# Optimization experiments

Measured on AMD Instinct MI355X. Metric: run time of the kernel, lower is better.

Reference implementation:

```python
import jax, jax.numpy as jnp
import numpy as np

EPS = 1e-5

def _layernorm(x, g, b):
    m = jnp.mean(x, axis=-1, keepdims=True)
    v = jnp.mean((x - m) ** 2, axis=-1, keepdims=True)
    return (x - m) * jax.lax.rsqrt(v + EPS) * g + b

def setup_inputs() -> dict:
    key = jax.random.key(0)
    ks = jax.random.split(key, 6)
    b, s, n = 1, 256, 512
    dim_msa, dim_pair, heads, dim_head = 64, 128, 8, 32
    dim_inner = heads * dim_head
    msa = jax.random.normal(ks[0], (b, s, n, dim_msa), dtype=jnp.float32)
    pairwise_repr = jax.random.normal(ks[1], (b, n, n, dim_pair), dtype=jnp.float32)
    mask = jnp.ones((b, n), dtype=bool)
    return {
        "msa": msa,
        "pairwise_repr": pairwise_repr,
        "ln_msa_g": jnp.ones((dim_msa,), jnp.float32),
        "ln_msa_b": jnp.zeros((dim_msa,), jnp.float32),
        "W_vg": jax.random.normal(ks[2], (dim_msa, dim_inner * 2), jnp.float32) * 0.02,
        "ln_pair_g": jnp.ones((dim_pair,), jnp.float32),
        "ln_pair_b": jnp.zeros((dim_pair,), jnp.float32),
        "W_pair": jax.random.normal(ks[3], (dim_pair, heads), jnp.float32) * 0.02,
        "W_out": jax.random.normal(ks[4], (dim_inner, dim_msa), jnp.float32) * 0.02,
        "mask": mask,
    }

def reference(msa, pairwise_repr, ln_msa_g, ln_msa_b, W_vg, ln_pair_g, ln_pair_b, W_pair, W_out, mask):
    heads, dim_head = 8, 32
    b, s, n, dim_msa = msa.shape
    # values and gates: LN -> LinearNoBias -> split (gv h d)
    vg = _layernorm(msa, ln_msa_g, ln_msa_b) @ W_vg            # [b,s,n,2*h*d]
    vg = vg.reshape(b, s, n, 2, heads, dim_head)
    vg = jnp.transpose(vg, (3, 0, 4, 1, 2, 5))                  # [2,b,h,s,n,d]
    values, gates = vg[0], jax.nn.sigmoid(vg[1])
    # pair bias: LN -> LinearNoBias -> [b,h,i,j]
    bias = _layernorm(pairwise_repr, ln_pair_g, ln_pair_b) @ W_pair  # [b,i,j,h]
    bias = jnp.transpose(bias, (0, 3, 1, 2))                    # [b,h,i,j]
    bias = jnp.where(mask[:, None, None, :], bias, -jnp.inf)
    weights = jax.nn.softmax(bias, axis=-1)                     # [b,h,i,j]
    out = jnp.einsum('bhij,bhsjd->bhsid', weights, values)      # [b,h,s,n,d]
    out = out * gates
    out = jnp.transpose(out, (0, 2, 3, 1, 4)).reshape(b, s, n, heads * dim_head)
    return out @ W_out                                          # [b,s,n,dim_msa]
```

## Files before the change

kernel.cpp:

```cpp
#include <hip/hip_runtime.h>
#include <hip/hip_bf16.h>


#define S 256
#define N 512
#define DM 64
#define DP 128
#define H 8
#define C 256
#define ROWS (S * N)

typedef __attribute__((ext_vector_type(8))) short bf16x8;
typedef __attribute__((ext_vector_type(4))) float f32x4;

static __device__ __forceinline__ float bf2f(unsigned int u16) {
    union { unsigned int i; float f; } x;
    x.i = u16 << 16;
    return x.f;
}
static __device__ __forceinline__ unsigned short f2bf(float f) {
    union { float f; unsigned int i; } x;
    x.f = f;
    unsigned int r = x.i + 0x7FFFu + ((x.i >> 16) & 1u);
    return (unsigned short)(r >> 16);
}
static __device__ __forceinline__ void gload16(const void* g, void* l) {
    __builtin_amdgcn_global_load_lds(
        (const __attribute__((address_space(1))) void*)g,
        (__attribute__((address_space(3))) void*)l, 16, 0, 0);
}

__global__ __launch_bounds__(256) void k0_prep(
    const float* __restrict__ Wvg, const float* __restrict__ g, const float* __restrict__ b,
    const float* __restrict__ Wout, const float* __restrict__ gp, const float* __restrict__ bp,
    const float* __restrict__ Wp,
    unsigned short* __restrict__ WTvg, float* __restrict__ biasvg, unsigned short* __restrict__ WoutT,
    float* __restrict__ Wg, float* __restrict__ sgcb)
{
    const int t = threadIdx.x;
    if (blockIdx.x < 2) {
        const int c = blockIdx.x * 256 + t;
        float bias = 0.f;
        unsigned short row[64];
#pragma unroll
        for (int k = 0; k < 64; k++) {
            const float w = Wvg[k * 512 + c];
            row[k] = f2bf(w * g[k]);
            bias = fmaf(w, b[k], bias);
        }
#pragma unroll
        for (int q = 0; q < 8; q++) *(uint4*)(WTvg + c * 64 + q * 8) = *(const uint4*)(row + q * 8);
        biasvg[c] = bias;
    } else if (blockIdx.x == 2) {
        const int m = t >> 2, c0 = (t & 3) * 64;
        unsigned short row[64];
#pragma unroll
        for (int q = 0; q < 64; q++) row[q] = f2bf(Wout[(c0 + q) * 64 + m]);
#pragma unroll
        for (int q = 0; q < 8; q++) *(uint4*)(WoutT + m * 256 + c0 + q * 8) = *(const uint4*)(row + q * 8);
    } else {
        if (t < 128) {
            const float gm = gp[t];
#pragma unroll
            for (int h = 0; h < 8; h++) Wg[t * 8 + h] = gm * Wp[t * 8 + h];
        } else if (t < 136) {
            const int h = t - 128;
            float sg = 0.f, cb = 0.f;
            for (int k = 0; k < 128; k++) {
                sg = fmaf(gp[k], Wp[k * 8 + h], sg);
                cb = fmaf(bp[k], Wp[k * 8 + h], cb);
            }
            sgcb[h] = sg;
            sgcb[8 + h] = cb;
        }
    }
}

__global__ __launch_bounds__(512, 4) void k1_vg_mfma(
    const float* __restrict__ msa, const unsigned short* __restrict__ WTvg,
    const float* __restrict__ biasvg,
    unsigned short* __restrict__ VT, unsigned short* __restrict__ G)
{
    __shared__ unsigned short wt[512 * 64];
    __shared__ unsigned short at[64 * 64];
    const int t = threadIdx.x, lane = t & 63, w = t >> 6;
    const int l15 = lane & 15, lgrp = lane >> 4;
    const int s = blockIdx.x >> 1;
    const int jbase = (blockIdx.x & 1) * 256;

#pragma unroll
    for (int q = 0; q < 8; q++) {
        const int u = q * 512 + t;
        const int c = u >> 3, ch = u & 7;
        const uint4 v = *(const uint4*)(WTvg + c * 64 + ch * 8);
        *(uint4*)((char*)wt + c * 128 + ((ch ^ (c & 7)) * 16)) = v;
    }
    float biasr[4];
    float bias2[4][4];
    if (w < 4) {
#pragma unroll
        for (int cf = 0; cf < 4; cf++) biasr[cf] = biasvg[w * 64 + cf * 16 + l15];
    } else {
#pragma unroll
        for (int cf = 0; cf < 4; cf++)
#pragma unroll
            for (int r = 0; r < 4; r++) bias2[cf][r] = biasvg[w * 64 + cf * 16 + lgrp * 4 + r];
    }

    for (int tile = 0; tile < 4; ++tile) {
        const int j0 = jbase + tile * 64;
        {
            const int r = t >> 3, kc = (t & 7) * 8;
            const float* src = msa + ((size_t)(s * 512 + j0 + r)) * 64 + kc;
            const float4 x0 = *(const float4*)src;
            const float4 x1 = *(const float4*)(src + 4);
            float s1 = x0.x + x0.y + x0.z + x0.w + x1.x + x1.y + x1.z + x1.w;
            float s2 = x0.x * x0.x + x0.y * x0.y + x0.z * x0.z + x0.w * x0.w
                     + x1.x * x1.x + x1.y * x1.y + x1.z * x1.z + x1.w * x1.w;
#pragma unroll
            for (int off = 1; off < 8; off <<= 1) {
                s1 += __shfl_xor(s1, off);
                s2 += __shfl_xor(s2, off);
            }
            const float m = s1 * (1.f / 64.f);
            const float inv = rsqrtf(s2 * (1.f / 64.f) - m * m + 1e-5f);
            unsigned short buf[8];
            buf[0] = f2bf((x0.x - m) * inv); buf[1] = f2bf((x0.y - m) * inv);
            buf[2] = f2bf((x0.z - m) * inv); buf[3] = f2bf((x0.w - m) * inv);
            buf[4] = f2bf((x1.x - m) * inv); buf[5] = f2bf((x1.y - m) * inv);
            buf[6] = f2bf((x1.z - m) * inv); buf[7] = f2bf((x1.w - m) * inv);
            *(uint4*)((char*)at + r * 128 + (((t & 7) ^ (r & 7)) * 16)) = *(const uint4*)buf;
        }
        __syncthreads();

        f32x4 acc[4][4];
#pragma unroll
        for (int rf = 0; rf < 4; rf++)
#pragma unroll
            for (int cf = 0; cf < 4; cf++) acc[rf][cf] = (f32x4){0.f, 0.f, 0.f, 0.f};

#pragma unroll
        for (int ks = 0; ks < 2; ks++) {
            bf16x8 bfr[4];
#pragma unroll
            for (int cf = 0; cf < 4; cf++) {
                const int c = w * 64 + cf * 16 + l15;
                bfr[cf] = *(const bf16x8*)((const char*)wt + c * 128 + (((ks * 4 + lgrp) ^ (c & 7)) * 16));
            }
#pragma unroll
            for (int rf = 0; rf < 4; rf++) {
                const int rr = rf * 16 + l15;
                const bf16x8 afr = *(const bf16x8*)((const char*)at + rr * 128 + (((ks * 4 + lgrp) ^ (rr & 7)) * 16));
                if (w < 4) {
#pragma unroll
                    for (int cf = 0; cf < 4; cf++)
                        acc[rf][cf] = __builtin_amdgcn_mfma_f32_16x16x32_bf16(afr, bfr[cf], acc[rf][cf], 0, 0, 0);
                } else {
#pragma unroll
                    for (int cf = 0; cf < 4; cf++)
                        acc[rf][cf] = __builtin_amdgcn_mfma_f32_16x16x32_bf16(bfr[cf], afr, acc[rf][cf], 0, 0, 0);
                }
            }
        }
        __syncthreads();

        if (w < 4) {
#pragma unroll
            for (int rf = 0; rf < 4; rf++)
#pragma unroll
                for (int cf = 0; cf < 4; cf++) {
                    const int c = w * 64 + cf * 16 + l15;
                    const int j = j0 + rf * 16 + lgrp * 4;
                    uint2 o;
                    o.x = (unsigned)f2bf(acc[rf][cf][0] + biasr[cf]) |
                          ((unsigned)f2bf(acc[rf][cf][1] + biasr[cf]) << 16);
                    o.y = (unsigned)f2bf(acc[rf][cf][2] + biasr[cf]) |
                          ((unsigned)f2bf(acc[rf][cf][3] + biasr[cf]) << 16);
                    *(uint2*)(VT + ((size_t)s * C + c) * N + j) = o;
                }
        } else {
#pragma unroll
            for (int rf = 0; rf < 4; rf++)
#pragma unroll
                for (int cf = 0; cf < 4; cf++) {
                    const int j = j0 + rf * 16 + l15;
                    const int cp = (w - 4) * 64 + cf * 16 + lgrp * 4;
                    float sg[4];
#pragma unroll
                    for (int r = 0; r < 4; r++)
                        sg[r] = 1.f / (1.f + __expf(-(acc[rf][cf][r] + bias2[cf][r])));
                    uint2 o;
                    o.x = (unsigned)f2bf(sg[0]) | ((unsigned)f2bf(sg[1]) << 16);
                    o.y = (unsigned)f2bf(sg[2]) | ((unsigned)f2bf(sg[3]) << 16);
                    *(uint2*)(G + ((size_t)(s * 512 + j)) * C + cp) = o;
                }
        }
    }
}

__global__ __launch_bounds__(512) void k2_bias_softmax(
    const float* __restrict__ pair, const float* __restrict__ Wg,
    const float* __restrict__ sgcb, unsigned short* __restrict__ Wt)
{
    __shared__ float bias_lds[H][N];
    const int i = blockIdx.x;
    const int t = threadIdx.x;
    const int sub = t & 15, rgrp = t >> 4;

    float wreg[2][4][8];
#pragma unroll
    for (int q = 0; q < 2; q++)
#pragma unroll
        for (int c = 0; c < 4; c++) {
            const int k = (q * 16 + sub) * 4 + c;
            const float4 w0 = *(const float4*)(Wg + k * 8);
            const float4 w1 = *(const float4*)(Wg + k * 8 + 4);
            wreg[q][c][0] = w0.x; wreg[q][c][1] = w0.y; wreg[q][c][2] = w0.z; wreg[q][c][3] = w0.w;
            wreg[q][c][4] = w1.x; wreg[q][c][5] = w1.y; wreg[q][c][6] = w1.z; wreg[q][c][7] = w1.w;
        }
    float sgr[8], cbr[8];
#pragma unroll
    for (int h = 0; h < 8; h++) { sgr[h] = sgcb[h]; cbr[h] = sgcb[8 + h]; }

    for (int pass = 0; pass < 16; ++pass) {
        const int r = pass * 32 + rgrp;
        const float* px = pair + ((size_t)i * N + r) * DP;
        const float4 x0 = *(const float4*)(px + (0 * 16 + sub) * 4);
        const float4 x1 = *(const float4*)(px + (1 * 16 + sub) * 4);
        float s1 = x0.x + x0.y + x0.z + x0.w + x1.x + x1.y + x1.z + x1.w;
        float s2 = x0.x * x0.x + x0.y * x0.y + x0.z * x0.z + x0.w * x0.w
                 + x1.x * x1.x + x1.y * x1.y + x1.z * x1.z + x1.w * x1.w;
#pragma unroll
        for (int off = 1; off < 16; off <<= 1) {
            s1 += __shfl_xor(s1, off);
            s2 += __shfl_xor(s2, off);
        }
        const float m = s1 * (1.f / 128.f);
        const float inv = rsqrtf(s2 * (1.f / 128.f) - m * m + 1e-5f);

        float dots[8];
#pragma unroll
        for (int h = 0; h < 8; h++) dots[h] = 0.f;
        const float xs[2][4] = {{x0.x, x0.y, x0.z, x0.w}, {x1.x, x1.y, x1.z, x1.w}};
#pragma unroll
        for (int q = 0; q < 2; q++)
#pragma unroll
            for (int c = 0; c < 4; c++)
#pragma unroll
                for (int h = 0; h < 8; h++) dots[h] = fmaf(xs[q][c], wreg[q][c][h], dots[h]);
#pragma unroll
        for (int off = 1; off < 16; off <<= 1)
#pragma unroll
            for (int h = 0; h < 8; h++) dots[h] += __shfl_xor(dots[h], off);

        if (sub == 0) {
#pragma unroll
            for (int h = 0; h < 8; h++)
                bias_lds[h][r] = inv * (dots[h] - m * sgr[h]) + cbr[h];
        }
    }
    __syncthreads();

    const int lane = t & 63, h = t >> 6;
    float v[8];
    float mx = -1e30f;
#pragma unroll
    for (int q = 0; q < 8; q++) {
        v[q] = bias_lds[h][q * 64 + lane];
        mx = fmaxf(mx, v[q]);
    }
#pragma unroll
    for (int off = 32; off > 0; off >>= 1) mx = fmaxf(mx, __shfl_xor(mx, off));
    float sum = 0.f;
#pragma unroll
    for (int q = 0; q < 8; q++) {
        v[q] = __expf(v[q] - mx);
        sum += v[q];
    }
#pragma unroll
    for (int off = 32; off > 0; off >>= 1) sum += __shfl_xor(sum, off);
    const float rs = 1.f / sum;
#pragma unroll
    for (int q = 0; q < 8; q++)
        Wt[((size_t)h * N + i) * N + q * 64 + lane] = f2bf(v[q] * rs);
}

__global__ __launch_bounds__(256, 2) void k3_einsum_h(
    const unsigned short* __restrict__ Wt, const unsigned short* __restrict__ VT,
    unsigned short* __restrict__ G)
{
    __shared__ unsigned short a_lds[2][128 * 64];
    __shared__ unsigned short b_lds[2][128 * 64];
    const int raw = blockIdx.x;
    const int bid = (raw & 7) * 256 + (raw >> 3);
    const int h = bid >> 8;
    const int rem = bid & 255;
    const int nb = rem >> 2, ib = rem & 3;
    const int n0 = nb * 128, i0 = ib * 128;
    const int t = threadIdx.x, lane = t & 63, w = t >> 6;
    const int l15 = lane & 15, lgrp = lane >> 4;
    const int wr = w >> 1, wc = w & 1;

    const unsigned short* srcA[4];
    const unsigned short* srcB[4];
    int dst[4];
#pragma unroll
    for (int q = 0; q < 4; ++q) {
        const int slot = q * 256 + t;
        const int row = slot >> 3, chp = slot & 7;
        const int ch = chp ^ (row & 7);
        const int n = n0 + row;
        srcA[q] = VT + ((size_t)((n >> 5) * 256 + h * 32 + (n & 31))) * 512 + ch * 8;
        srcB[q] = Wt + ((size_t)(h * 512 + i0 + row)) * 512 + ch * 8;
        dst[q] = slot * 16;
    }

#define K3_STAGE(P, J0)                                                    \
    {                                                                      \
        _Pragma("unroll")                                                  \
        for (int q = 0; q < 4; ++q)                                        \
            gload16(srcA[q] + (J0), (char*)a_lds[P] + dst[q]);             \
        _Pragma("unroll")                                                  \
        for (int q = 0; q < 4; ++q)                                        \
            gload16(srcB[q] + (J0), (char*)b_lds[P] + dst[q]);             \
    }

    f32x4 acc[4][4];
#pragma unroll
    for (int fn = 0; fn < 4; fn++)
#pragma unroll
        for (int fi = 0; fi < 4; fi++) acc[fn][fi] = (f32x4){0.f, 0.f, 0.f, 0.f};

    K3_STAGE(0, 0);

    for (int kt = 0; kt < 8; ++kt) {
        const int cur = kt & 1;
        if (kt < 7) {
            K3_STAGE(cur ^ 1, (kt + 1) * 64);
            asm volatile("s_waitcnt vmcnt(8)" ::: "memory");
        } else {
            asm volatile("s_waitcnt vmcnt(0)" ::: "memory");
        }
        __builtin_amdgcn_s_barrier();
#pragma unroll
        for (int ks = 0; ks < 2; ++ks) {
            bf16x8 af[4], bf[4];
#pragma unroll
            for (int f = 0; f < 4; ++f) {
                const int ra = wr * 64 + f * 16 + l15;
                af[f] = *(const bf16x8*)((const char*)a_lds[cur] + ra * 128 + (((ks * 4 + lgrp) ^ (ra & 7)) * 16));
                const int rb = wc * 64 + f * 16 + l15;
                bf[f] = *(const bf16x8*)((const char*)b_lds[cur] + rb * 128 + (((ks * 4 + lgrp) ^ (rb & 7)) * 16));
            }
#pragma unroll
            for (int fn = 0; fn < 4; ++fn)
#pragma unroll
                for (int fi = 0; fi < 4; ++fi)
                    acc[fn][fi] = __builtin_amdgcn_mfma_f32_16x16x32_bf16(af[fn], bf[fi], acc[fn][fi], 0, 0, 0);
        }
        __builtin_amdgcn_s_barrier();
    }
#undef K3_STAGE

#pragma unroll
    for (int fn = 0; fn < 4; ++fn) {
        const int nl = n0 + wr * 64 + fn * 16 + lgrp * 4;
        const int s = nl >> 5, d = nl & 31;
#pragma unroll
        for (int fi = 0; fi < 4; ++fi) {
            const int i = i0 + wc * 64 + fi * 16 + l15;
            const size_t base = ((size_t)(s * 512 + i)) * 256 + h * 32 + d;
            const uint2 u = *(const uint2*)(G + base);
            const float g0 = bf2f(u.x & 0xFFFFu), g1 = bf2f(u.x >> 16);
            const float g2 = bf2f(u.y & 0xFFFFu), g3 = bf2f(u.y >> 16);
            uint2 o;
            o.x = (unsigned)f2bf(acc[fn][fi][0] * g0) | ((unsigned)f2bf(acc[fn][fi][1] * g1) << 16);
            o.y = (unsigned)f2bf(acc[fn][fi][2] * g2) | ((unsigned)f2bf(acc[fn][fi][3] * g3) << 16);
            *(uint2*)(G + base) = o;
        }
    }
}

__global__ __launch_bounds__(256, 4) void k4_out(
    const unsigned short* __restrict__ gated, const unsigned short* __restrict__ WoutT,
    float* __restrict__ out)
{
    __shared__ unsigned short w_lds[64 * 256];
    __shared__ unsigned short a_lds[64 * 256];
    const int t = threadIdx.x, lane = t & 63, w = t >> 6;
    const int l15 = lane & 15, lgrp = lane >> 4;
    const size_t r0 = (size_t)blockIdx.x * 64;

#pragma unroll
    for (int q = 0; q < 8; ++q) {
        const int u = q * 256 + t;
        const int row = u >> 5, kc = u & 31;
        const uint4 v = *(const uint4*)(WoutT + row * 256 + kc * 8);
        *(uint4*)((char*)w_lds + row * 512 + ((kc ^ (row & 31)) * 16)) = v;
    }
#pragma unroll
    for (int q = 0; q < 8; ++q) {
        const int slot = q * 256 + t;
        const int row = slot >> 5, chp = slot & 31;
        const int ch = chp ^ (row & 31);
        gload16(gated + (r0 + row) * 256 + ch * 8,
                (char*)a_lds + (q * 256 + (t & 192)) * 16);
    }
    __syncthreads();

    f32x4 acc[4];
#pragma unroll
    for (int fm = 0; fm < 4; fm++) acc[fm] = (f32x4){0.f, 0.f, 0.f, 0.f};
#pragma unroll
    for (int ks = 0; ks < 8; ++ks) {
        const int ra = w * 16 + l15;
        const bf16x8 af = *(const bf16x8*)((const char*)a_lds + ra * 512 + (((ks * 4 + lgrp) ^ (ra & 31)) * 16));
#pragma unroll
        for (int fm = 0; fm < 4; ++fm) {
            const int rm = fm * 16 + l15;
            const bf16x8 bf = *(const bf16x8*)((const char*)w_lds + rm * 512 + (((ks * 4 + lgrp) ^ (rm & 31)) * 16));
            acc[fm] = __builtin_amdgcn_mfma_f32_16x16x32_bf16(af, bf, acc[fm], 0, 0, 0);
        }
    }
#pragma unroll
    for (int fm = 0; fm < 4; ++fm)
#pragma unroll
        for (int r = 0; r < 4; ++r)
            out[(r0 + w * 16 + lgrp * 4 + r) * 64 + fm * 16 + l15] = acc[fm][r];
}

extern "C" void kernel_launch(void* const* d_in, const int* in_sizes, int n_in,
                              void* d_out, int out_size, void* d_ws, size_t ws_size,
                              hipStream_t stream) {
    (void)in_sizes; (void)n_in; (void)out_size; (void)ws_size;
    const float* msa       = (const float*)d_in[0];
    const float* pair      = (const float*)d_in[1];
    const float* ln_msa_g  = (const float*)d_in[2];
    const float* ln_msa_b  = (const float*)d_in[3];
    const float* W_vg      = (const float*)d_in[4];
    const float* ln_pair_g = (const float*)d_in[5];
    const float* ln_pair_b = (const float*)d_in[6];
    const float* W_pair    = (const float*)d_in[7];
    const float* W_out     = (const float*)d_in[8];
    float* out = (float*)d_out;

    char* ws = (char*)d_ws;
    size_t off = 0;
    unsigned short* VT    = (unsigned short*)(ws + off); off += (size_t)ROWS * C * 2;
    unsigned short* G     = (unsigned short*)(ws + off); off += (size_t)ROWS * C * 2;
    unsigned short* Wt    = (unsigned short*)(ws + off); off += (size_t)H * N * N * 2;
    unsigned short* WTvg  = (unsigned short*)(ws + off); off += 512 * 64 * 2;
    float*          biasvg = (float*)(ws + off); off += 512 * 4;
    unsigned short* WoutT = (unsigned short*)(ws + off); off += 64 * 256 * 2;
    float*          Wg    = (float*)(ws + off); off += 128 * 8 * 4;
    float*          sgcb  = (float*)(ws + off); off += 16 * 4;

    k0_prep<<<4, 256, 0, stream>>>(W_vg, ln_msa_g, ln_msa_b, W_out, ln_pair_g, ln_pair_b, W_pair,
                                   WTvg, biasvg, WoutT, Wg, sgcb);
    k1_vg_mfma<<<512, 512, 0, stream>>>(msa, WTvg, biasvg, VT, G);
    k2_bias_softmax<<<512, 512, 0, stream>>>(pair, Wg, sgcb, Wt);
    k3_einsum_h<<<2048, 256, 0, stream>>>(Wt, VT, G);
    k4_out<<<2048, 256, 0, stream>>>(G, WoutT, out);
}
```

Baseline: 215.8 us.

## Loop all heads inside each einsum block to reuse VT/G spatial locality

The einsum kernel now assigns each block two s-rows by 128 i-columns and iterates over all 8 heads in a 64-step pipelined loop, writing gated output per head. Gate values are prefetched at the start of each head. The grid shrinks from 2048 to 512 blocks and the A tile halves, so each block has less MFMA work per step but a longer pipeline. The softmax kernel is also launched before the value/gate projection, so VT and G are likely still in cache when the einsum reads them. The risk is lower parallelism (512 blocks) and more per-head epilogue stalls.

```diff
diff --git a/kernel.cpp b/kernel.cpp
--- a/kernel.cpp
+++ b/kernel.cpp
@@ -289,96 +289,127 @@
     const unsigned short* __restrict__ Wt, const unsigned short* __restrict__ VT,
     unsigned short* __restrict__ G)
 {
-    __shared__ unsigned short a_lds[2][128 * 64];
+    __shared__ unsigned short a_lds[2][64 * 64];
     __shared__ unsigned short b_lds[2][128 * 64];
     const int raw = blockIdx.x;
-    const int bid = (raw & 7) * 256 + (raw >> 3);
-    const int h = bid >> 8;
-    const int rem = bid & 255;
-    const int nb = rem >> 2, ib = rem & 3;
-    const int n0 = nb * 128, i0 = ib * 128;
+    const int bid = (raw & 7) * 64 + (raw >> 3);
+    const int nb = bid >> 2;
+    const int ib = bid & 3;
+    const int s0 = nb * 2;
+    const int i0 = ib * 128;
     const int t = threadIdx.x, lane = t & 63, w = t >> 6;
     const int l15 = lane & 15, lgrp = lane >> 4;
     const int wr = w >> 1, wc = w & 1;
 
-    const unsigned short* srcA[4];
+    const unsigned short* srcA[2];
     const unsigned short* srcB[4];
-    int dst[4];
+    int dstA[2], dstB[4];
+#pragma unroll
+    for (int q = 0; q < 2; ++q) {
+        const int slot = q * 256 + t;
+        const int row = slot >> 3, chp = slot & 7;
+        const int ch = chp ^ (row & 7);
+        const int s = s0 + (row >> 5);
+        srcA[q] = VT + ((size_t)(s * 256 + (row & 31))) * 512 + ch * 8;
+        dstA[q] = slot * 16;
+    }
 #pragma unroll
     for (int q = 0; q < 4; ++q) {
         const int slot = q * 256 + t;
         const int row = slot >> 3, chp = slot & 7;
         const int ch = chp ^ (row & 7);
-        const int n = n0 + row;
-        srcA[q] = VT + ((size_t)((n >> 5) * 256 + h * 32 + (n & 31))) * 512 + ch * 8;
-        srcB[q] = Wt + ((size_t)(h * 512 + i0 + row)) * 512 + ch * 8;
-        dst[q] = slot * 16;
-    }
-
-#define K3_STAGE(P, J0)                                                    \
-    {                                                                      \
-        _Pragma("unroll")                                                  \
-        for (int q = 0; q < 4; ++q)                                        \
-            gload16(srcA[q] + (J0), (char*)a_lds[P] + dst[q]);             \
-        _Pragma("unroll")                                                  \
-        for (int q = 0; q < 4; ++q)                                        \
-            gload16(srcB[q] + (J0), (char*)b_lds[P] + dst[q]);             \
-    }
-
-    f32x4 acc[4][4];
-#pragma unroll
-    for (int fn = 0; fn < 4; fn++)
+        srcB[q] = Wt + ((size_t)(i0 + row)) * 512 + ch * 8;
+        dstB[q] = slot * 16;
+    }
+
+#define K3_STAGE(P, U)                                                          \
+    {                                                                           \
+        const int hh_ = (U) >> 3, kk_ = (U) & 7;                                \
+        const int offA_ = hh_ * 16384 + kk_ * 64;                               \
+        const int offB_ = hh_ * 262144 + kk_ * 64;                              \
+        _Pragma("unroll")                                                       \
+        for (int q = 0; q < 2; ++q) gload16(srcA[q] + offA_, (char*)a_lds[P] + dstA[q]); \
+        _Pragma("unroll")                                                       \
+        for (int q = 0; q < 4; ++q) gload16(srcB[q] + offB_, (char*)b_lds[P] + dstB[q]); \
+    }
+
+    f32x4 acc[2][4];
+#pragma unroll
+    for (int fn = 0; fn < 2; fn++)
 #pragma unroll
         for (int fi = 0; fi < 4; fi++) acc[fn][fi] = (f32x4){0.f, 0.f, 0.f, 0.f};
+    uint2 gpre[2][4];
 
     K3_STAGE(0, 0);
 
-    for (int kt = 0; kt < 8; ++kt) {
-        const int cur = kt & 1;
-        if (kt < 7) {
-            K3_STAGE(cur ^ 1, (kt + 1) * 64);
-            asm volatile("s_waitcnt vmcnt(8)" ::: "memory");
+    for (int u = 0; u < 64; ++u) {
+        const int cur = u & 1;
+        if (u < 63) {
+            K3_STAGE(cur ^ 1, u + 1);
+            asm volatile("s_waitcnt vmcnt(6)" ::: "memory");
         } else {
             asm volatile("s_waitcnt vmcnt(0)" ::: "memory");
         }
         __builtin_amdgcn_s_barrier();
+
+        if ((u & 7) == 0) {
+            const int h = u >> 3;
+#pragma unroll
+            for (int fn = 0; fn < 2; ++fn) {
+                const int nl = wr * 32 + fn * 16 + lgrp * 4;
+                const int s = s0 + (nl >> 5), d = nl & 31;
+#pragma unroll
+                for (int fi = 0; fi < 4; ++fi) {
+                    const int i = i0 + wc * 64 + fi * 16 + l15;
+                    gpre[fn][fi] = *(const uint2*)(G + ((size_t)(s * 512 + i)) * 256 + h * 32 + d);
+                }
+            }
+        }
+
 #pragma unroll
         for (int ks = 0; ks < 2; ++ks) {
-            bf16x8 af[4], bf[4];
+            bf16x8 af[2], bf[4];
+#pragma unroll
+            for (int f = 0; f < 2; ++f) {
+                const int ra = wr * 32 + f * 16 + l15;
+                af[f] = *(const bf16x8*)((const char*)a_lds[cur] + ra * 128 + (((ks * 4 + lgrp) ^ (ra & 7)) * 16));
+            }
 #pragma unroll
             for (int f = 0; f < 4; ++f) {
-                const int ra = wr * 64 + f * 16 + l15;
-                af[f] = *(const bf16x8*)((const char*)a_lds[cur] + ra * 128 + (((ks * 4 + lgrp) ^ (ra & 7)) * 16));
                 const int rb = wc * 64 + f * 16 + l15;
                 bf[f] = *(const bf16x8*)((const char*)b_lds[cur] + rb * 128 + (((ks * 4 + lgrp) ^ (rb & 7)) * 16));
             }
 #pragma unroll
-            for (int fn = 0; fn < 4; ++fn)
+            for (int fn = 0; fn < 2; ++fn)
 #pragma unroll
                 for (int fi = 0; fi < 4; ++fi)
                     acc[fn][fi] = __builtin_amdgcn_mfma_f32_16x16x32_bf16(af[fn], bf[fi], acc[fn][fi], 0, 0, 0);
         }
         __builtin_amdgcn_s_barrier();
+
+        if ((u & 7) == 7) {
+            const int h = u >> 3;
+#pragma unroll
+            for (int fn = 0; fn < 2; ++fn) {
+                const int nl = wr * 32 + fn * 16 + lgrp * 4;
+                const int s = s0 + (nl >> 5), d = nl & 31;
+#pragma unroll
+                for (int fi = 0; fi < 4; ++fi) {
+                    const int i = i0 + wc * 64 + fi * 16 + l15;
+                    const size_t base = ((size_t)(s * 512 + i)) * 256 + h * 32 + d;
+                    const uint2 uu = gpre[fn][fi];
+                    const float g0 = bf2f(uu.x & 0xFFFFu), g1 = bf2f(uu.x >> 16);
+                    const float g2 = bf2f(uu.y & 0xFFFFu), g3 = bf2f(uu.y >> 16);
+                    uint2 o;
+                    o.x = (unsigned)f2bf(acc[fn][fi][0] * g0) | ((unsigned)f2bf(acc[fn][fi][1] * g1) << 16);
+                    o.y = (unsigned)f2bf(acc[fn][fi][2] * g2) | ((unsigned)f2bf(acc[fn][fi][3] * g3) << 16);
+                    *(uint2*)(G + base) = o;
+                    acc[fn][fi] = (f32x4){0.f, 0.f, 0.f, 0.f};
+                }
+            }
+        }
     }
 #undef K3_STAGE
-
-#pragma unroll
-    for (int fn = 0; fn < 4; ++fn) {
-        const int nl = n0 + wr * 64 + fn * 16 + lgrp * 4;
-        const int s = nl >> 5, d = nl & 31;
-#pragma unroll
-        for (int fi = 0; fi < 4; ++fi) {
-            const int i = i0 + wc * 64 + fi * 16 + l15;
-            const size_t base = ((size_t)(s * 512 + i)) * 256 + h * 32 + d;
-            const uint2 u = *(const uint2*)(G + base);
-            const float g0 = bf2f(u.x & 0xFFFFu), g1 = bf2f(u.x >> 16);
-            const float g2 = bf2f(u.y & 0xFFFFu), g3 = bf2f(u.y >> 16);
-            uint2 o;
-            o.x = (unsigned)f2bf(acc[fn][fi][0] * g0) | ((unsigned)f2bf(acc[fn][fi][1] * g1) << 16);
-            o.y = (unsigned)f2bf(acc[fn][fi][2] * g2) | ((unsigned)f2bf(acc[fn][fi][3] * g3) << 16);
-            *(uint2*)(G + base) = o;
-        }
-    }
 }
 
 __global__ __launch_bounds__(256, 4) void k4_out(
@@ -457,8 +488,8 @@
 
     k0_prep<<<4, 256, 0, stream>>>(W_vg, ln_msa_g, ln_msa_b, W_out, ln_pair_g, ln_pair_b, W_pair,
                                    WTvg, biasvg, WoutT, Wg, sgcb);
+    k2_bias_softmax<<<512, 512, 0, stream>>>(pair, Wg, sgcb, Wt);
     k1_vg_mfma<<<512, 512, 0, stream>>>(msa, WTvg, biasvg, VT, G);
-    k2_bias_softmax<<<512, 512, 0, stream>>>(pair, Wg, sgcb, Wt);
-    k3_einsum_h<<<2048, 256, 0, stream>>>(Wt, VT, G);
+    k3_einsum_h<<<512, 256, 0, stream>>>(Wt, VT, G);
     k4_out<<<2048, 256, 0, stream>>>(G, WoutT, out);
 }
```

New measurement: 224.4 us. 1.04x slower.

## Enlarge einsum tile to 128x256 and drop double buffering in k3

Applied to the files above, without the earlier changes.

The einsum kernel now computes a 128(n) x 256(i) tile per block instead of 128x128, so each V tile is reused across twice as many output columns and the grid halves to 1024 blocks. LDS double buffering is replaced by a single-buffer load/sync/compute/sync loop with 48KB LDS, and each wave holds 4x8 accumulator fragments. The softmax kernel is also launched before the vg projection. Register pressure rises (128 accumulator floats per lane) and losing the prefetch overlap may expose global load latency, since launch_bounds still asks for 2 blocks per CU.

```diff
diff --git a/kernel.cpp b/kernel.cpp
--- a/kernel.cpp
+++ b/kernel.cpp
@@ -289,21 +289,21 @@
     const unsigned short* __restrict__ Wt, const unsigned short* __restrict__ VT,
     unsigned short* __restrict__ G)
 {
-    __shared__ unsigned short a_lds[2][128 * 64];
-    __shared__ unsigned short b_lds[2][128 * 64];
+    __shared__ unsigned short a_lds[128 * 64];
+    __shared__ unsigned short b_lds[256 * 64];
     const int raw = blockIdx.x;
-    const int bid = (raw & 7) * 256 + (raw >> 3);
-    const int h = bid >> 8;
-    const int rem = bid & 255;
-    const int nb = rem >> 2, ib = rem & 3;
-    const int n0 = nb * 128, i0 = ib * 128;
+    const int bid = (raw & 7) * 128 + (raw >> 3);
+    const int h = bid >> 7;
+    const int rem = bid & 127;
+    const int nb = rem >> 1, ib = rem & 1;
+    const int n0 = nb * 128, i0 = ib * 256;
     const int t = threadIdx.x, lane = t & 63, w = t >> 6;
     const int l15 = lane & 15, lgrp = lane >> 4;
-    const int wr = w >> 1, wc = w & 1;
+    const int wn = w >> 1, wi = w & 1;
 
     const unsigned short* srcA[4];
-    const unsigned short* srcB[4];
-    int dst[4];
+    const unsigned short* srcB[8];
+    int dstA[4], dstB[8];
 #pragma unroll
     for (int q = 0; q < 4; ++q) {
         const int slot = q * 256 + t;
@@ -311,68 +311,65 @@
         const int ch = chp ^ (row & 7);
         const int n = n0 + row;
         srcA[q] = VT + ((size_t)((n >> 5) * 256 + h * 32 + (n & 31))) * 512 + ch * 8;
+        dstA[q] = slot * 16;
+    }
+#pragma unroll
+    for (int q = 0; q < 8; ++q) {
+        const int slot = q * 256 + t;
+        const int row = slot >> 3, chp = slot & 7;
+        const int ch = chp ^ (row & 7);
         srcB[q] = Wt + ((size_t)(h * 512 + i0 + row)) * 512 + ch * 8;
-        dst[q] = slot * 16;
-    }
-
-#define K3_STAGE(P, J0)                                                    \
-    {                                                                      \
-        _Pragma("unroll")                                                  \
-        for (int q = 0; q < 4; ++q)                                        \
-            gload16(srcA[q] + (J0), (char*)a_lds[P] + dst[q]);             \
-        _Pragma("unroll")                                                  \
-        for (int q = 0; q < 4; ++q)                                        \
-            gload16(srcB[q] + (J0), (char*)b_lds[P] + dst[q]);             \
-    }
-
-    f32x4 acc[4][4];
+        dstB[q] = slot * 16;
+    }
+
+    f32x4 acc[4][8];
 #pragma unroll
     for (int fn = 0; fn < 4; fn++)
 #pragma unroll
-        for (int fi = 0; fi < 4; fi++) acc[fn][fi] = (f32x4){0.f, 0.f, 0.f, 0.f};
-
-    K3_STAGE(0, 0);
+        for (int fi = 0; fi < 8; fi++) acc[fn][fi] = (f32x4){0.f, 0.f, 0.f, 0.f};
 
     for (int kt = 0; kt < 8; ++kt) {
-        const int cur = kt & 1;
-        if (kt < 7) {
-            K3_STAGE(cur ^ 1, (kt + 1) * 64);
-            asm volatile("s_waitcnt vmcnt(8)" ::: "memory");
-        } else {
-            asm volatile("s_waitcnt vmcnt(0)" ::: "memory");
-        }
-        __builtin_amdgcn_s_barrier();
+        const int j0 = kt * 64;
+#pragma unroll
+        for (int q = 0; q < 4; ++q) gload16(srcA[q] + j0, (char*)a_lds + dstA[q]);
+#pragma unroll
+        for (int q = 0; q < 8; ++q) gload16(srcB[q] + j0, (char*)b_lds + dstB[q]);
+        __syncthreads();
+
 #pragma unroll
         for (int ks = 0; ks < 2; ++ks) {
-            bf16x8 af[4], bf[4];
-#pragma unroll
-            for (int f = 0; f < 4; ++f) {
-                const int ra = wr * 64 + f * 16 + l15;
-                af[f] = *(const bf16x8*)((const char*)a_lds[cur] + ra * 128 + (((ks * 4 + lgrp) ^ (ra & 7)) * 16));
-                const int rb = wc * 64 + f * 16 + l15;
-                bf[f] = *(const bf16x8*)((const char*)b_lds[cur] + rb * 128 + (((ks * 4 + lgrp) ^ (rb & 7)) * 16));
+            bf16x8 af[4];
+#pragma unroll
+            for (int fn = 0; fn < 4; ++fn) {
+                const int ra = wn * 64 + fn * 16 + l15;
+                af[fn] = *(const bf16x8*)((const char*)a_lds + ra * 128 + (((ks * 4 + lgrp) ^ (ra & 7)) * 16));
+            }
+            bf16x8 bf[8];
+#pragma unroll
+            for (int fi = 0; fi < 8; ++fi) {
+                const int rb = wi * 128 + fi * 16 + l15;
+                bf[fi] = *(const bf16x8*)((const char*)b_lds + rb * 128 + (((ks * 4 + lgrp) ^ (rb & 7)) * 16));
             }
 #pragma unroll
             for (int fn = 0; fn < 4; ++fn)
 #pragma unroll
-                for (int fi = 0; fi < 4; ++fi)
+                for (int fi = 0; fi < 8; ++fi)
                     acc[fn][fi] = __builtin_amdgcn_mfma_f32_16x16x32_bf16(af[fn], bf[fi], acc[fn][fi], 0, 0, 0);
         }
-        __builtin_amdgcn_s_barrier();
-    }
-#undef K3_STAGE
+        __syncthreads();
+    }
 
 #pragma unroll
     for (int fn = 0; fn < 4; ++fn) {
-        const int nl = n0 + wr * 64 + fn * 16 + lgrp * 4;
+        const int nl = n0 + wn * 64 + fn * 16 + lgrp * 4;
         const int s = nl >> 5, d = nl & 31;
 #pragma unroll
-        for (int fi = 0; fi < 4; ++fi) {
-            const int i = i0 + wc * 64 + fi * 16 + l15;
+        for (int fi = 0; fi < 8; ++fi) {
+            const int i = i0 + wi * 128 + fi * 16 + l15;
             const size_t base = ((size_t)(s * 512 + i)) * 256 + h * 32 + d;
-            const uint2 u = *(const uint2*)(G + base);
-            const float g0 = bf2f(u.x & 0xFFFFu), g1 = bf2f(u.x >> 16);
-            const float g2 = bf2f(u.y & 0xFFFFu), g3 = bf2f(u.y >> 16);
+            const uint2 uu = *(const uint2*)(G + base);
+            const float g0 = bf2f(uu.x & 0xFFFFu), g1 = bf2f(uu.x >> 16);
+            const float g2 = bf2f(uu.y & 0xFFFFu), g3 = bf2f(uu.y >> 16);
             uint2 o;
             o.x = (unsigned)f2bf(acc[fn][fi][0] * g0) | ((unsigned)f2bf(acc[fn][fi][1] * g1) << 16);
             o.y = (unsigned)f2bf(acc[fn][fi][2] * g2) | ((unsigned)f2bf(acc[fn][fi][3] * g3) << 16);
@@ -457,8 +454,8 @@
 
     k0_prep<<<4, 256, 0, stream>>>(W_vg, ln_msa_g, ln_msa_b, W_out, ln_pair_g, ln_pair_b, W_pair,
                                    WTvg, biasvg, WoutT, Wg, sgcb);
+    k2_bias_softmax<<<512, 512, 0, stream>>>(pair, Wg, sgcb, Wt);
     k1_vg_mfma<<<512, 512, 0, stream>>>(msa, WTvg, biasvg, VT, G);
-    k2_bias_softmax<<<512, 512, 0, stream>>>(pair, Wg, sgcb, Wt);
-    k3_einsum_h<<<2048, 256, 0, stream>>>(Wt, VT, G);
+    k3_einsum_h<<<1024, 256, 0, stream>>>(Wt, VT, G);
     k4_out<<<2048, 256, 0, stream>>>(G, WoutT, out);
 }
```

Result: slower. 227.0 us (+5.2%).
